# Performance work log

Measured on AMD Instinct MI355X. Metric: run time of the kernel, lower is better.

The kernel has to match this reference:

```python
import jax, jax.numpy as jnp
import numpy as np

N = 100000      # nodes
E = 1600000     # edges
F_IN = 256      # input features
HID = 64        # hidden channels
C = 10          # classes
EPS = 0.3       # FAGCN epsilon (raw-feature residual scale)
NUM_LAYERS = 2


def setup_inputs() -> dict:
    key = jax.random.key(0)
    ks = jax.random.split(key, 8)
    x = jax.random.normal(ks[0], (N, F_IN), dtype=jnp.float32)
    edge_index = jax.random.randint(ks[1], (2, E), 0, N, dtype=jnp.int32)
    # lin1 / lin2 (xavier-normal-ish scale)
    w1 = jax.random.normal(ks[2], (HID, F_IN), dtype=jnp.float32) * (1.414 / np.sqrt(F_IN))
    b1 = jnp.zeros((HID,), dtype=jnp.float32)
    w2 = jax.random.normal(ks[3], (C, HID), dtype=jnp.float32) * (1.414 / np.sqrt(HID))
    b2 = jnp.zeros((C,), dtype=jnp.float32)
    # per-layer FAConv attention vectors att_l, att_r: [NUM_LAYERS, HID]
    att_l = jax.random.normal(ks[4], (NUM_LAYERS, HID), dtype=jnp.float32) * (1.0 / np.sqrt(HID))
    att_r = jax.random.normal(ks[5], (NUM_LAYERS, HID), dtype=jnp.float32) * (1.0 / np.sqrt(HID))
    return {"x": x, "edge_index": edge_index, "w1": w1, "b1": b1,
            "w2": w2, "b2": b2, "att_l": att_l, "att_r": att_r}


def reference(x, edge_index, w1, b1, w2, b2, att_l, att_r):
    src = edge_index[0]  # [E] message source j
    dst = edge_index[1]  # [E] aggregation target i

    # gcn_norm without self-loops: deg from destination, symmetric normalization
    deg = jax.ops.segment_sum(jnp.ones((E,), x.dtype), dst, num_segments=N)
    dis = jnp.where(deg > 0, jax.lax.rsqrt(jnp.maximum(deg, 1.0)), 0.0)
    norm = dis[src] * dis[dst]  # [E]

    h = jax.nn.relu(x @ w1.T + b1)  # [N, HID]
    raw = h
    for l in range(NUM_LAYERS):
        al = h @ att_l[l]  # [N] per-node left score
        ar = h @ att_r[l]  # [N] per-node right score
        # alpha_j (att_l at source) + alpha_i (att_r at destination)
        alpha = jnp.tanh(al[src] + ar[dst])  # [E]
        msg = h[src] * (alpha * norm)[:, None]  # [E, HID]
        agg = jax.ops.segment_sum(msg, dst, num_segments=N)  # [N, HID]
        h = agg + EPS * raw

    logits = h @ w2.T + b2  # [N, C]
    return jax.nn.log_softmax(logits, axis=1)
```

## Files before the change

kernel.cpp:

```cpp
#include <hip/hip_runtime.h>

#define NN 100000
#define NE 1600000
#define FIN 256
#define HID 64
#define NCLS 10
#define EPSF 0.3f


__global__ void k_wt(const float* __restrict__ w1, float* __restrict__ w1T) {
    int t = blockIdx.x * 256 + threadIdx.x;
    if (t < HID * FIN) {
        int k = t >> 6;
        int h = t & 63;
        w1T[t] = w1[h * FIN + k];
    }
}

__global__ void k_deg(const int* __restrict__ ei, int* __restrict__ deg) {
    int e = blockIdx.x * 256 + threadIdx.x;
    if (e < NE) atomicAdd(&deg[ei[NE + e]], 1);
}

__global__ void k_dis(const int* __restrict__ deg, float* __restrict__ dis) {
    int i = blockIdx.x * 256 + threadIdx.x;
    if (i < NN) {
        int d = deg[i];
        dis[i] = (d > 0) ? (1.0f / sqrtf((float)d)) : 0.0f;
    }
}

__global__ void k_scan1(const int* __restrict__ deg, int* __restrict__ rp, int* __restrict__ bsum) {
    __shared__ int s[1024];
    int i = blockIdx.x * 1024 + threadIdx.x;
    int v = (i < NN) ? deg[i] : 0;
    s[threadIdx.x] = v;
    __syncthreads();
    for (int off = 1; off < 1024; off <<= 1) {
        int t = (threadIdx.x >= off) ? s[threadIdx.x - off] : 0;
        __syncthreads();
        s[threadIdx.x] += t;
        __syncthreads();
    }
    if (i < NN) rp[i] = s[threadIdx.x] - v;
    if (threadIdx.x == 1023) bsum[blockIdx.x] = s[1023];
}

__global__ void k_scan2(int* __restrict__ bsum, int nb) {
    __shared__ int s[128];
    int v = (threadIdx.x < nb) ? bsum[threadIdx.x] : 0;
    s[threadIdx.x] = v;
    __syncthreads();
    for (int off = 1; off < 128; off <<= 1) {
        int t = (threadIdx.x >= off) ? s[threadIdx.x - off] : 0;
        __syncthreads();
        s[threadIdx.x] += t;
        __syncthreads();
    }
    if (threadIdx.x < nb) bsum[threadIdx.x] = s[threadIdx.x] - v;
}

__global__ void k_scan3(int* __restrict__ rp, const int* __restrict__ bsum) {
    int i = blockIdx.x * 1024 + threadIdx.x;
    if (i < NN) rp[i] += bsum[blockIdx.x];
    if (i == 0) rp[NN] = NE;
}

__global__ void k_fill(const int* __restrict__ ei, const int* __restrict__ rp,
                       int* __restrict__ cursor, int* __restrict__ csr_src) {
    int e = blockIdx.x * 256 + threadIdx.x;
    if (e < NE) {
        int s = ei[e], d = ei[NE + e];
        int pos = rp[d] + atomicAdd(&cursor[d], 1);
        csr_src[pos] = s;
    }
}


__global__ __launch_bounds__(256) void k_gemm1(const float* __restrict__ x, const float* __restrict__ w1T,
                                               const float* __restrict__ b1, const float* __restrict__ dis,
                                               const float* __restrict__ att_l0, const float* __restrict__ att_r0,
                                               float* __restrict__ h,
                                               float2* __restrict__ aldis, float2* __restrict__ ardis) {
    __shared__ float4 wlds[FIN * (HID / 4)];
    const float4* __restrict__ wr = reinterpret_cast<const float4*>(w1T);
    for (int t = threadIdx.x; t < FIN * (HID / 4); t += 256) wlds[t] = wr[t];
    __syncthreads();

    int n = blockIdx.x * 256 + threadIdx.x;
    bool act = (n < NN);
    int nc = act ? n : (NN - 1);
    float acc[HID];
#pragma unroll
    for (int j = 0; j < HID; j++) acc[j] = b1[j];
    const float4* __restrict__ xr = reinterpret_cast<const float4*>(x + (size_t)nc * FIN);

    float4 cur = xr[0];
#pragma unroll 1
    for (int k4 = 0; k4 < FIN / 4; k4++) {
        float4 nxt = make_float4(0.f, 0.f, 0.f, 0.f);
        if (k4 < FIN / 4 - 1) nxt = xr[k4 + 1];
        const float* xf = &cur.x;
#pragma unroll
        for (int kk = 0; kk < 4; kk++) {
            float xs = xf[kk];
            const float4* wrow = &wlds[(k4 * 4 + kk) * (HID / 4)];
#pragma unroll
            for (int hq = 0; hq < HID / 4; hq++) {
                float4 wq = wrow[hq];
                acc[hq * 4 + 0] = fmaf(xs, wq.x, acc[hq * 4 + 0]);
                acc[hq * 4 + 1] = fmaf(xs, wq.y, acc[hq * 4 + 1]);
                acc[hq * 4 + 2] = fmaf(xs, wq.z, acc[hq * 4 + 2]);
                acc[hq * 4 + 3] = fmaf(xs, wq.w, acc[hq * 4 + 3]);
            }
        }
        cur = nxt;
    }

    if (!act) return;
    float4* __restrict__ ho = reinterpret_cast<float4*>(h + (size_t)n * HID);
    float p = 0.0f, q = 0.0f;
#pragma unroll
    for (int hq = 0; hq < HID / 4; hq++) {
        float4 v;
        v.x = fmaxf(acc[hq * 4 + 0], 0.0f);
        v.y = fmaxf(acc[hq * 4 + 1], 0.0f);
        v.z = fmaxf(acc[hq * 4 + 2], 0.0f);
        v.w = fmaxf(acc[hq * 4 + 3], 0.0f);
        ho[hq] = v;
        p = fmaf(v.x, att_l0[hq * 4 + 0], p); q = fmaf(v.x, att_r0[hq * 4 + 0], q);
        p = fmaf(v.y, att_l0[hq * 4 + 1], p); q = fmaf(v.y, att_r0[hq * 4 + 1], q);
        p = fmaf(v.z, att_l0[hq * 4 + 2], p); q = fmaf(v.z, att_r0[hq * 4 + 2], q);
        p = fmaf(v.w, att_l0[hq * 4 + 3], p); q = fmaf(v.w, att_r0[hq * 4 + 3], q);
    }
    float ds = dis[n];
    aldis[n] = make_float2(p, ds);
    ardis[n] = make_float2(q, ds);
}

template <int MODE>
__global__ __launch_bounds__(256) void k_agg(const float* __restrict__ h_in, const float* __restrict__ raw,
                                             const int* __restrict__ rp, const int* __restrict__ csr_src,
                                             const float2* __restrict__ aldis_i, const float2* __restrict__ ardis_i,
                                             float* __restrict__ h_out,
                                             const float* __restrict__ att_l, const float* __restrict__ att_r,
                                             const float* __restrict__ dis,
                                             float2* __restrict__ aldis_o, float2* __restrict__ ardis_o,
                                             const float* __restrict__ w2, const float* __restrict__ b2,
                                             float* __restrict__ out) {
    int lane = threadIdx.x & 63;
    int i = blockIdx.x * 4 + (threadIdx.x >> 6);
    if (i >= NN) return;
    float2 ai = ardis_i[i];
    float acc = EPSF * raw[(size_t)i * HID + lane];
    int e0 = rp[i], e1 = rp[i + 1];
    int deg = e1 - e0;
    float a0 = 0.0f, a1 = 0.0f, a2 = 0.0f, a3 = 0.0f;
    for (int base = 0; base < deg; base += 64) {
        int rem = deg - base; if (rem > 64) rem = 64;
        int j = 0; float cf = 0.0f;
        if (lane < rem) {
            j = csr_src[e0 + base + lane];
            float2 aj = aldis_i[j];
            cf = tanhf(aj.x + ai.x) * (aj.y * ai.y);
        }
        int t = 0;
        for (; t + 4 <= rem; t += 4) {
            int j0 = __shfl(j, t, 64), j1 = __shfl(j, t + 1, 64);
            int j2 = __shfl(j, t + 2, 64), j3 = __shfl(j, t + 3, 64);
            float c0 = __shfl(cf, t, 64), c1 = __shfl(cf, t + 1, 64);
            float c2 = __shfl(cf, t + 2, 64), c3 = __shfl(cf, t + 3, 64);
            float h0 = h_in[(size_t)j0 * HID + lane];
            float h1 = h_in[(size_t)j1 * HID + lane];
            float h2 = h_in[(size_t)j2 * HID + lane];
            float h3 = h_in[(size_t)j3 * HID + lane];
            a0 = fmaf(h0, c0, a0);
            a1 = fmaf(h1, c1, a1);
            a2 = fmaf(h2, c2, a2);
            a3 = fmaf(h3, c3, a3);
        }
        for (; t < rem; ++t) {
            int jj = __shfl(j, t, 64);
            float cc = __shfl(cf, t, 64);
            a0 = fmaf(h_in[(size_t)jj * HID + lane], cc, a0);
        }
    }
    acc += (a0 + a1) + (a2 + a3);

    if (MODE == 2) {
        float lg[NCLS];
#pragma unroll
        for (int cc = 0; cc < NCLS; cc++) {
            float p = acc * w2[cc * HID + lane];
#pragma unroll
            for (int m = 1; m < 64; m <<= 1) p += __shfl_xor(p, m, 64);
            lg[cc] = p + b2[cc];
        }
        float mx = lg[0];
#pragma unroll
        for (int cc = 1; cc < NCLS; cc++) mx = fmaxf(mx, lg[cc]);
        float ssum = 0.0f;
#pragma unroll
        for (int cc = 0; cc < NCLS; cc++) ssum += expf(lg[cc] - mx);
        float r = mx + logf(ssum);
        if (lane < NCLS) {
            float v = 0.0f;
#pragma unroll
            for (int cc = 0; cc < NCLS; cc++)
                if (lane == cc) v = lg[cc];
            out[(size_t)i * NCLS + lane] = v - r;
        }
    } else {
        h_out[(size_t)i * HID + lane] = acc;
        if (MODE == 1) {
            float p = acc * att_l[lane];
            float q = acc * att_r[lane];
#pragma unroll
            for (int m = 1; m < 64; m <<= 1) {
                p += __shfl_xor(p, m, 64);
                q += __shfl_xor(q, m, 64);
            }
            if (lane == 0) {
                float ds = dis[i];
                aldis_o[i] = make_float2(p, ds);
                ardis_o[i] = make_float2(q, ds);
            }
        }
    }
}


extern "C" void kernel_launch(void* const* d_in, const int* in_sizes, int n_in,
                              void* d_out, int out_size, void* d_ws, size_t ws_size,
                              hipStream_t stream) {
    const float* x     = (const float*)d_in[0];
    const int*   ei    = (const int*)d_in[1];
    const float* w1    = (const float*)d_in[2];
    const float* b1    = (const float*)d_in[3];
    const float* w2    = (const float*)d_in[4];
    const float* b2    = (const float*)d_in[5];
    const float* att_l = (const float*)d_in[6];
    const float* att_r = (const float*)d_in[7];
    float* out = (float*)d_out;

    char* ws = (char*)d_ws;
    size_t off = 0;
    auto take = [&](size_t bytes) -> void* {
        void* p = ws + off;
        off += (bytes + 255) & ~(size_t)255;
        return p;
    };
    int*    deg     = (int*)take((size_t)NN * 4);
    int*    cursor  = (int*)take((size_t)NN * 4);
    int*    rp      = (int*)take((size_t)(NN + 1) * 4);
    int*    bsum    = (int*)take(128 * 4);
    float*  dis     = (float*)take((size_t)NN * 4);
    float2* aldisA  = (float2*)take((size_t)NN * 8);
    float2* ardisA  = (float2*)take((size_t)NN * 8);
    float2* aldisB  = (float2*)take((size_t)NN * 8);
    float2* ardisB  = (float2*)take((size_t)NN * 8);
    float*  w1T     = (float*)take((size_t)HID * FIN * 4);
    int*    csr_src = (int*)take((size_t)NE * 4);
    float*  hA      = (float*)take((size_t)NN * HID * 4);
    float*  hB      = (float*)take((size_t)NN * HID * 4);

    hipMemsetAsync(deg, 0, (size_t)NN * 4, stream);
    hipMemsetAsync(cursor, 0, (size_t)NN * 4, stream);

    const int EB = (NE + 255) / 256;
    const int NB = (NN + 255) / 256;
    const int SB = (NN + 1023) / 1024;

    k_wt<<<64, 256, 0, stream>>>(w1, w1T);
    k_deg<<<EB, 256, 0, stream>>>(ei, deg);
    k_dis<<<NB, 256, 0, stream>>>(deg, dis);
    k_scan1<<<SB, 1024, 0, stream>>>(deg, rp, bsum);
    k_scan2<<<1, 128, 0, stream>>>(bsum, SB);
    k_scan3<<<SB, 1024, 0, stream>>>(rp, bsum);
    k_fill<<<EB, 256, 0, stream>>>(ei, rp, cursor, csr_src);

    k_gemm1<<<(NN + 255) / 256, 256, 0, stream>>>(x, w1T, b1, dis, att_l, att_r, hA, aldisA, ardisA);

    k_agg<1><<<NN / 4, 256, 0, stream>>>(hA, hA, rp, csr_src, aldisA, ardisA, hB,
                                         att_l + HID, att_r + HID, dis, aldisB, ardisB,
                                         nullptr, nullptr, nullptr);

    k_agg<2><<<NN / 4, 256, 0, stream>>>(hB, hA, rp, csr_src, aldisB, ardisB, nullptr,
                                         nullptr, nullptr, nullptr, nullptr, nullptr,
                                         w2, b2, out);
}
```

Measured before the change: 557.0 us.

## Gather neighbor rows with float4 loads, four edges per wavefront step

Restructures the per-node aggregation so that each wavefront splits into four 16-lane groups. Each lane loads a float4 of a neighbor's feature row, so one wavefront handles eight edges per iteration instead of issuing a scalar load per edge. Partial sums are combined across groups with xor shuffles, and the epilogue dot products (attention scores and the classifier) are reduced over 16 lanes. This cuts the number of load instructions and shuffles per edge, at the cost of wasted lanes when degree is not a multiple of eight and an extra cross-group reduction.

```diff
diff --git a/kernel.cpp b/kernel.cpp
--- a/kernel.cpp
+++ b/kernel.cpp
@@ -149,13 +149,17 @@
                                              const float* __restrict__ w2, const float* __restrict__ b2,
                                              float* __restrict__ out) {
     int lane = threadIdx.x & 63;
+    int g = lane >> 4;
+    int f = lane & 15;
     int i = blockIdx.x * 4 + (threadIdx.x >> 6);
     if (i >= NN) return;
     float2 ai = ardis_i[i];
-    float acc = EPSF * raw[(size_t)i * HID + lane];
     int e0 = rp[i], e1 = rp[i + 1];
     int deg = e1 - e0;
-    float a0 = 0.0f, a1 = 0.0f, a2 = 0.0f, a3 = 0.0f;
+
+    float4 accA = make_float4(0.f, 0.f, 0.f, 0.f);
+    float4 accB = make_float4(0.f, 0.f, 0.f, 0.f);
+
     for (int base = 0; base < deg; base += 64) {
         int rem = deg - base; if (rem > 64) rem = 64;
         int j = 0; float cf = 0.0f;
@@ -164,36 +168,55 @@
             float2 aj = aldis_i[j];
             cf = tanhf(aj.x + ai.x) * (aj.y * ai.y);
         }
-        int t = 0;
-        for (; t + 4 <= rem; t += 4) {
-            int j0 = __shfl(j, t, 64), j1 = __shfl(j, t + 1, 64);
-            int j2 = __shfl(j, t + 2, 64), j3 = __shfl(j, t + 3, 64);
-            float c0 = __shfl(cf, t, 64), c1 = __shfl(cf, t + 1, 64);
-            float c2 = __shfl(cf, t + 2, 64), c3 = __shfl(cf, t + 3, 64);
-            float h0 = h_in[(size_t)j0 * HID + lane];
-            float h1 = h_in[(size_t)j1 * HID + lane];
-            float h2 = h_in[(size_t)j2 * HID + lane];
-            float h3 = h_in[(size_t)j3 * HID + lane];
-            a0 = fmaf(h0, c0, a0);
-            a1 = fmaf(h1, c1, a1);
-            a2 = fmaf(h2, c2, a2);
-            a3 = fmaf(h3, c3, a3);
-        }
-        for (; t < rem; ++t) {
-            int jj = __shfl(j, t, 64);
-            float cc = __shfl(cf, t, 64);
-            a0 = fmaf(h_in[(size_t)jj * HID + lane], cc, a0);
-        }
-    }
-    acc += (a0 + a1) + (a2 + a3);
+        for (int t = 0; t < rem; t += 8) {
+            int i0 = t + g;
+            int i1 = t + 4 + g;
+            int s0 = i0 < rem ? i0 : rem - 1;
+            int s1 = i1 < rem ? i1 : rem - 1;
+            int j0 = __shfl(j, s0, 64);
+            int j1 = __shfl(j, s1, 64);
+            float c0 = __shfl(cf, s0, 64);
+            float c1 = __shfl(cf, s1, 64);
+            if (i0 >= rem) c0 = 0.0f;
+            if (i1 >= rem) c1 = 0.0f;
+            float4 h0 = *reinterpret_cast<const float4*>(h_in + j0 * HID + 4 * f);
+            float4 h1 = *reinterpret_cast<const float4*>(h_in + j1 * HID + 4 * f);
+            accA.x = fmaf(h0.x, c0, accA.x);
+            accA.y = fmaf(h0.y, c0, accA.y);
+            accA.z = fmaf(h0.z, c0, accA.z);
+            accA.w = fmaf(h0.w, c0, accA.w);
+            accB.x = fmaf(h1.x, c1, accB.x);
+            accB.y = fmaf(h1.y, c1, accB.y);
+            accB.z = fmaf(h1.z, c1, accB.z);
+            accB.w = fmaf(h1.w, c1, accB.w);
+        }
+    }
+    float4 acc;
+    acc.x = accA.x + accB.x;
+    acc.y = accA.y + accB.y;
+    acc.z = accA.z + accB.z;
+    acc.w = accA.w + accB.w;
+#pragma unroll
+    for (int m = 16; m <= 32; m <<= 1) {
+        acc.x += __shfl_xor(acc.x, m, 64);
+        acc.y += __shfl_xor(acc.y, m, 64);
+        acc.z += __shfl_xor(acc.z, m, 64);
+        acc.w += __shfl_xor(acc.w, m, 64);
+    }
+    float4 rawv = *reinterpret_cast<const float4*>(raw + (size_t)i * HID + 4 * f);
+    acc.x = fmaf(EPSF, rawv.x, acc.x);
+    acc.y = fmaf(EPSF, rawv.y, acc.y);
+    acc.z = fmaf(EPSF, rawv.z, acc.z);
+    acc.w = fmaf(EPSF, rawv.w, acc.w);
 
     if (MODE == 2) {
         float lg[NCLS];
 #pragma unroll
         for (int cc = 0; cc < NCLS; cc++) {
-            float p = acc * w2[cc * HID + lane];
-#pragma unroll
-            for (int m = 1; m < 64; m <<= 1) p += __shfl_xor(p, m, 64);
+            float4 wv = *reinterpret_cast<const float4*>(w2 + cc * HID + 4 * f);
+            float p = acc.x * wv.x + acc.y * wv.y + acc.z * wv.z + acc.w * wv.w;
+#pragma unroll
+            for (int m = 1; m < 16; m <<= 1) p += __shfl_xor(p, m, 64);
             lg[cc] = p + b2[cc];
         }
         float mx = lg[0];
@@ -211,12 +234,14 @@
             out[(size_t)i * NCLS + lane] = v - r;
         }
     } else {
-        h_out[(size_t)i * HID + lane] = acc;
+        if (g == 0) *reinterpret_cast<float4*>(h_out + (size_t)i * HID + 4 * f) = acc;
         if (MODE == 1) {
-            float p = acc * att_l[lane];
-            float q = acc * att_r[lane];
-#pragma unroll
-            for (int m = 1; m < 64; m <<= 1) {
+            float4 alv = *reinterpret_cast<const float4*>(att_l + 4 * f);
+            float4 arv = *reinterpret_cast<const float4*>(att_r + 4 * f);
+            float p = acc.x * alv.x + acc.y * alv.y + acc.z * alv.z + acc.w * alv.w;
+            float q = acc.x * arv.x + acc.y * arv.y + acc.z * arv.z + acc.w * arv.w;
+#pragma unroll
+            for (int m = 1; m < 16; m <<= 1) {
                 p += __shfl_xor(p, m, 64);
                 q += __shfl_xor(q, m, 64);
             }
```

After: 536.9 us. 1.04x faster.
